# Performance work log

Measured on AMD Instinct MI355X. Metric: run time of the kernel, lower is better.

Reference implementation:

```python
import jax, jax.numpy as jnp
import numpy as np

H = 8  # num_heads


def setup_inputs() -> dict:
    key = jax.random.key(0)
    ks = jax.random.split(key, 8)
    B, N, C = 2048, 64, 256  # B = batch(8) * nW(256) windows, N = window tokens, C = dim
    nW = 256
    return {
        "x": jax.random.normal(ks[0], (B, N, C), jnp.float32),
        "mask": jax.random.normal(ks[1], (nW, N, N), jnp.float32),
        "Wq": jax.random.normal(ks[2], (C, C), jnp.float32) * (C ** -0.5),
        "bq": jax.random.normal(ks[3], (C,), jnp.float32) * 0.02,
        "Wkv": jax.random.normal(ks[4], (C, 2 * C), jnp.float32) * (C ** -0.5),
        "bkv": jax.random.normal(ks[5], (2 * C,), jnp.float32) * 0.02,
        "Wp": jax.random.normal(ks[6], (C, C), jnp.float32) * (C ** -0.5),
        "bp": jax.random.normal(ks[7], (C,), jnp.float32) * 0.02,
    }


def reference(x, mask, Wq, bq, Wkv, bkv, Wp, bp):
    B, N, C = x.shape
    dh = C // H
    scale = dh ** -0.5
    # projections (attn_kv is None -> self-attention)
    q = (x @ Wq + bq).reshape(B, N, H, dh).transpose(0, 2, 1, 3)          # [B,H,N,dh]
    kv = (x @ Wkv + bkv).reshape(B, N, 2, H, dh).transpose(2, 0, 3, 1, 4)  # [2,B,H,N,dh]
    k, v = kv[0], kv[1]
    attn = jnp.einsum("bhqd,bhkd->bhqk", q * scale, k)                    # [B,H,N,N]
    nW = mask.shape[0]
    attn = attn.reshape(B // nW, nW, H, N, N) + mask[None, :, None]
    attn = attn.reshape(B, H, N, N)
    attn = jax.nn.softmax(attn, axis=-1)
    out = jnp.einsum("bhqk,bhkd->bhqd", attn, v)                          # [B,H,N,dh]
    out = out.transpose(0, 2, 1, 3).reshape(B, N, C)
    return out @ Wp + bp
```

## Files before the change

kernel.cpp:

```cpp
#include <hip/hip_runtime.h>

typedef __bf16 bf16v8 __attribute__((ext_vector_type(8)));
typedef bf16v8 bf16x8 __attribute__((may_alias));
typedef unsigned int u32v2 __attribute__((ext_vector_type(2)));
typedef u32v2 u32x2 __attribute__((may_alias));
typedef unsigned short u16v8 __attribute__((ext_vector_type(8)));
typedef u16v8 u16x8 __attribute__((may_alias));
typedef unsigned short u16v;
typedef u16v u16 __attribute__((may_alias));
typedef _Float16 f16v4 __attribute__((ext_vector_type(4)));
typedef f16v4 f16x4 __attribute__((may_alias));
typedef _Float16 f16v;
typedef f16v f16s __attribute__((may_alias));
typedef float f32x4 __attribute__((ext_vector_type(4)));
typedef unsigned int u32;

#define MEMFENCE() asm volatile("" ::: "memory")

union B8 { u32 u[4]; bf16v8 v; };

__device__ __forceinline__ u32 cvtpk(float lo, float hi) {
    u32 r;
    asm("v_cvt_pk_bf16_f32 %0, %1, %2" : "=v"(r) : "v"(lo), "v"(hi));
    return r;
}

__device__ __forceinline__ unsigned short f2b(float f) {
    union { float f; unsigned u; } a; a.f = f;
    unsigned r = a.u + 0x7FFFu + ((a.u >> 16) & 1u);
    return (unsigned short)(r >> 16);
}

__global__ void prep_weights(const float* __restrict__ Wq,
                             const float* __restrict__ Wkv,
                             const float* __restrict__ Wp,
                             const float* __restrict__ bq,
                             const float* __restrict__ bkv,
                             u16* __restrict__ wt,
                             u16* __restrict__ wpt,
                             float* __restrict__ b_all)
{
    int idx = blockIdx.x * 256 + threadIdx.x;
    if (idx < 196608) {
        int h  = idx / 24576;   int r  = idx % 24576;
        int m  = r / 8192;      int r2 = r % 8192;
        int tj = r2 / 4096;     int r3 = r2 % 4096;
        int ks = r3 / 512;      int r4 = r3 % 512;
        int lane = r4 >> 3, j = r4 & 7;
        int o = h * 32 + tj * 16 + (lane & 15);
        int k = ks * 32 + (lane >> 4) * 8 + j;
        float v = (m == 0) ? Wq[k * 256 + o]
                           : Wkv[k * 512 + (m == 1 ? o : 256 + o)];
        wt[idx] = f2b(v);
    } else if (idx < 262144) {
        int f  = idx - 196608;
        int h  = f / 8192;      int r2 = f % 8192;
        int tj = r2 / 4096;     int r3 = r2 % 4096;
        int ks = r3 / 512;      int r4 = r3 % 512;
        int lane = r4 >> 3, j = r4 & 7;
        int o = h * 32 + tj * 16 + (lane & 15);
        int k = ks * 32 + (lane >> 4) * 8 + j;
        wpt[f] = f2b(Wp[k * 256 + o]);
    } else if (idx < 262912) {
        int i = idx - 262144;
        b_all[i] = (i < 256) ? bq[i] : bkv[i - 256];
    }
}

__global__ __launch_bounds__(512, 2)
void qkv_proj(const float* __restrict__ x,
              const u16* __restrict__ wt,
              const float* __restrict__ b_all,
              u16* __restrict__ qkv)
{
    __shared__ __align__(16) unsigned char smem[32768];
    const int b   = blockIdx.x;
    const int tid = threadIdx.x;
    const int w   = tid >> 6;
    const int l   = tid & 63;
    const int lr  = l & 15;
    const int lg  = l >> 4;
    const int hc  = w * 32;

    f32x4 zero = {0.f, 0.f, 0.f, 0.f};

    {
        const float* xb = x + (size_t)b * 16384;
#pragma unroll
        for (int it = 0; it < 4; ++it) {
            int g   = it * 512 + tid;
            int row = g >> 5;
            int cg  = g & 31;
            const float4 f0 = *(const float4*)(xb + row * 256 + cg * 8);
            const float4 f1 = *(const float4*)(xb + row * 256 + cg * 8 + 4);
            u16v8 t;
            t[0] = f2b(f0.x); t[1] = f2b(f0.y); t[2] = f2b(f0.z); t[3] = f2b(f0.w);
            t[4] = f2b(f1.x); t[5] = f2b(f1.y); t[6] = f2b(f1.z); t[7] = f2b(f1.w);
            int off = row * 512 + ((cg * 16) ^ ((row & 7) << 4));
            *(u16x8*)(smem + off) = t;
        }
    }
    __syncthreads();

    u16* qb  = qkv + (((size_t)b * 8 + w) * 3) * 2048;
    u16* kb_ = qb + 2048;
    unsigned char* vb = (unsigned char*)(qb + 4096);
    const u16* whead = wt + (size_t)w * 24576;

#pragma unroll
    for (int hf = 0; hf < 2; ++hf) {
        f32x4 qa[2][2], ka[2][2], va[2][2];
#pragma unroll
        for (int t = 0; t < 2; ++t)
#pragma unroll
            for (int tj = 0; tj < 2; ++tj) { qa[t][tj] = zero; ka[t][tj] = zero; va[t][tj] = zero; }
#pragma unroll
        for (int ks = 0; ks < 8; ++ks) {
            bf16v8 af[2];
#pragma unroll
            for (int t = 0; t < 2; ++t) {
                int row = hf * 32 + t * 16 + lr;
                af[t] = *(const bf16x8*)(smem + row * 512 + ((ks * 64 + lg * 16) ^ ((row & 7) << 4)));
            }
            bf16v8 bwq[2], bwk[2], bwv[2];
#pragma unroll
            for (int tj = 0; tj < 2; ++tj) {
                const u16* wp0 = whead + tj * 4096 + ks * 512 + l * 8;
                bwq[tj] = *(const bf16x8*)(wp0);
                bwk[tj] = *(const bf16x8*)(wp0 + 8192);
                bwv[tj] = *(const bf16x8*)(wp0 + 16384);
            }
            __builtin_amdgcn_s_setprio(1);
#pragma unroll
            for (int tj = 0; tj < 2; ++tj)
#pragma unroll
                for (int t = 0; t < 2; ++t) {
                    qa[t][tj] = __builtin_amdgcn_mfma_f32_16x16x32_bf16(af[t], bwq[tj], qa[t][tj], 0, 0, 0);
                    ka[t][tj] = __builtin_amdgcn_mfma_f32_16x16x32_bf16(af[t], bwk[tj], ka[t][tj], 0, 0, 0);
                    va[t][tj] = __builtin_amdgcn_mfma_f32_16x16x32_bf16(af[t], bwv[tj], va[t][tj], 0, 0, 0);
                }
            __builtin_amdgcn_s_setprio(0);
        }
#pragma unroll
        for (int tj = 0; tj < 2; ++tj) {
            float bqv = b_all[hc + tj * 16 + lr];
            float bkr = b_all[256 + hc + tj * 16 + lr];
            float bvr = b_all[512 + hc + tj * 16 + lr];
#pragma unroll
            for (int t = 0; t < 2; ++t) {
#pragma unroll
                for (int e = 0; e < 4; ++e) {
                    int tok = hf * 32 + t * 16 + lg * 4 + e;
                    qb[tok * 32 + tj * 16 + lr]  = f2b(qa[t][tj][e] + bqv);
                    kb_[tok * 32 + tj * 16 + lr] = f2b(ka[t][tj][e] + bkr);
                }
                int dh   = tj * 16 + lr;
                int tok0 = hf * 32 + t * 16 + lg * 4;
                u32x2 pv2;
                pv2[0] = cvtpk(va[t][tj][0] + bvr, va[t][tj][1] + bvr);
                pv2[1] = cvtpk(va[t][tj][2] + bvr, va[t][tj][3] + bvr);
                *(u32x2*)(vb + dh * 128 + tok0 * 2) = pv2;
            }
        }
    }
}

__global__ __launch_bounds__(512, 4)
void attn_out(const u16* __restrict__ qkv,
              const float* __restrict__ mask,
              const u16* __restrict__ wpt,
              const float* __restrict__ bp,
              float* __restrict__ out)
{
    __shared__ __align__(16) unsigned char smem[40960];
    const int b   = blockIdx.x;
    const int wdw = b & 255;
    const int tid = threadIdx.x;
    const int w   = tid >> 6;
    const int l   = tid & 63;
    const int lr  = l & 15;
    const int lg  = l >> 4;
    const int chunk = w * 4096;
    const int moff  = 32768;
    const int hc    = w * 32;
    const float scale = 0.17677669529663687f;

    f32x4 zero = {0.f, 0.f, 0.f, 0.f};

    {
        const float* mb = mask + (size_t)wdw * 4096;
#pragma unroll
        for (int it = 0; it < 8; ++it) {
            int idx = it * 512 + tid;
            int q = idx >> 6, k = idx & 63;
            int colp = (k & 15) * 4 + (k >> 4);
            *(f16s*)(smem + moff + q * 128 + ((colp * 2) ^ ((q & 7) << 4)))
                = (_Float16)mb[idx];
        }
    }
    __syncthreads();

    const u16* qb  = qkv + (((size_t)b * 8 + w) * 3) * 2048;
    const u16* kb_ = qb + 2048;
    const unsigned char* vb = (const unsigned char*)(qb + 4096);

    bf16v8 aq[4], bk[4];
#pragma unroll
    for (int ti = 0; ti < 4; ++ti)
        aq[ti] = *(const bf16x8*)(qb + (ti * 16 + lr) * 32 + lg * 8);
#pragma unroll
    for (int tj = 0; tj < 4; ++tj)
        bk[tj] = *(const bf16x8*)(kb_ + (tj * 16 + lr) * 32 + lg * 8);

    f32x4 sH[4][4];
    __builtin_amdgcn_s_setprio(1);
#pragma unroll
    for (int ti = 0; ti < 4; ++ti)
#pragma unroll
        for (int tj = 0; tj < 4; ++tj)
            sH[ti][tj] = __builtin_amdgcn_mfma_f32_16x16x32_bf16(aq[ti], bk[tj], zero, 0, 0, 0);
    __builtin_amdgcn_s_setprio(0);

#pragma unroll
    for (int ti = 0; ti < 4; ++ti)
#pragma unroll
        for (int e = 0; e < 4; ++e) {
            int row = ti * 16 + lg * 4 + e;
            f16v4 mv = *(const f16x4*)(smem + moff + row * 128 + ((lr * 8) ^ ((row & 7) << 4)));
#pragma unroll
            for (int tj = 0; tj < 4; ++tj)
                sH[ti][tj][e] = sH[ti][tj][e] * scale + (float)mv[tj];
        }
    float inv[4][4];
#pragma unroll
    for (int ti = 0; ti < 4; ++ti)
#pragma unroll
        for (int e = 0; e < 4; ++e) {
            float v0 = sH[ti][0][e], v1 = sH[ti][1][e];
            float v2 = sH[ti][2][e], v3 = sH[ti][3][e];
            float m = fmaxf(fmaxf(v0, v1), fmaxf(v2, v3));
#pragma unroll
            for (int d = 1; d < 16; d <<= 1) m = fmaxf(m, __shfl_xor(m, d));
            v0 = __expf(v0 - m); v1 = __expf(v1 - m);
            v2 = __expf(v2 - m); v3 = __expf(v3 - m);
            float s = v0 + v1 + v2 + v3;
#pragma unroll
            for (int d = 1; d < 16; d <<= 1) s += __shfl_xor(s, d);
            inv[ti][e] = 1.0f / s;
            sH[ti][0][e] = v0; sH[ti][1][e] = v1;
            sH[ti][2][e] = v2; sH[ti][3][e] = v3;
        }
    u32 pkP[4][4][2];
#pragma unroll
    for (int ti = 0; ti < 4; ++ti)
#pragma unroll
        for (int tj = 0; tj < 4; ++tj) {
            pkP[ti][tj][0] = cvtpk(sH[ti][tj][0], sH[ti][tj][1]);
            pkP[ti][tj][1] = cvtpk(sH[ti][tj][2], sH[ti][tj][3]);
        }

    f32x4 oH[4][2];
#pragma unroll
    for (int ti = 0; ti < 4; ++ti)
#pragma unroll
        for (int tjv = 0; tjv < 2; ++tjv) oH[ti][tjv] = zero;
#pragma unroll
    for (int kb2 = 0; kb2 < 2; ++kb2) {
#pragma unroll
        for (int ti = 0; ti < 4; ++ti)
#pragma unroll
            for (int tjh = 0; tjh < 2; ++tjh) {
                int c2 = (tjh * 16 + lr) * 2;
#pragma unroll
                for (int ep = 0; ep < 2; ++ep) {
                    u32 u = pkP[ti][2 * kb2 + tjh][ep];
                    int q0 = ti * 16 + lg * 4 + ep * 2;
                    *(u16*)(smem + chunk + q0 * 64 + (c2 ^ (((q0 >> 1) & 3) << 4))) = (unsigned short)u;
                    *(u16*)(smem + chunk + (q0 + 1) * 64 + (c2 ^ ((((q0 + 1) >> 1) & 3) << 4))) = (unsigned short)(u >> 16);
                }
            }
        MEMFENCE();
        bf16v8 bv[2];
#pragma unroll
        for (int tjv = 0; tjv < 2; ++tjv) {
            int dh = tjv * 16 + lr;
            bv[tjv] = *(const bf16x8*)(vb + dh * 128 + kb2 * 64 + lg * 16);
        }
#pragma unroll
        for (int ti = 0; ti < 4; ++ti) {
            int row = ti * 16 + lr;
            bf16v8 ap = *(const bf16x8*)(smem + chunk + row * 64 + ((lg * 16) ^ (((row >> 1) & 3) << 4)));
            __builtin_amdgcn_s_setprio(1);
#pragma unroll
            for (int tjv = 0; tjv < 2; ++tjv)
                oH[ti][tjv] = __builtin_amdgcn_mfma_f32_16x16x32_bf16(ap, bv[tjv], oH[ti][tjv], 0, 0, 0);
            __builtin_amdgcn_s_setprio(0);
        }
        MEMFENCE();
    }
#pragma unroll
    for (int ti = 0; ti < 4; ++ti)
#pragma unroll
        for (int tjv = 0; tjv < 2; ++tjv)
#pragma unroll
            for (int e = 0; e < 4; ++e)
                oH[ti][tjv][e] *= inv[ti][e];

    __syncthreads();

#pragma unroll
    for (int ti = 0; ti < 4; ++ti)
#pragma unroll
        for (int tjv = 0; tjv < 2; ++tjv)
#pragma unroll
            for (int e = 0; e < 4; ++e) {
                int row = ti * 16 + lg * 4 + e;
                int cg  = hc + tjv * 16 + lr;
                *(u16*)(smem + row * 512 + ((cg * 2) ^ ((row & 7) << 4)))
                    = f2b(oH[ti][tjv][e]);
            }
    __syncthreads();

    f32x4 pacc[4][2];
#pragma unroll
    for (int ti = 0; ti < 4; ++ti)
#pragma unroll
        for (int tj = 0; tj < 2; ++tj) pacc[ti][tj] = zero;
#pragma unroll
    for (int ks = 0; ks < 8; ++ks) {
        bf16v8 a_[4];
#pragma unroll
        for (int ti = 0; ti < 4; ++ti) {
            int row = ti * 16 + lr;
            a_[ti] = *(const bf16x8*)(smem + row * 512 + ((ks * 64 + lg * 16) ^ ((row & 7) << 4)));
        }
        bf16v8 bw[2];
#pragma unroll
        for (int tj = 0; tj < 2; ++tj)
            bw[tj] = *(const bf16x8*)(wpt + (size_t)w * 8192 + tj * 4096 + ks * 512 + l * 8);
        __builtin_amdgcn_s_setprio(1);
#pragma unroll
        for (int tj = 0; tj < 2; ++tj)
#pragma unroll
            for (int ti = 0; ti < 4; ++ti)
                pacc[ti][tj] = __builtin_amdgcn_mfma_f32_16x16x32_bf16(a_[ti], bw[tj], pacc[ti][tj], 0, 0, 0);
        __builtin_amdgcn_s_setprio(0);
    }
    float* ob = out + (size_t)b * 16384;
#pragma unroll
    for (int tj = 0; tj < 2; ++tj) {
        float bias = bp[hc + tj * 16 + lr];
#pragma unroll
        for (int ti = 0; ti < 4; ++ti)
#pragma unroll
            for (int e = 0; e < 4; ++e) {
                int row = ti * 16 + lg * 4 + e;
                ob[row * 256 + hc + tj * 16 + lr] = pacc[ti][tj][e] + bias;
            }
    }
}

extern "C" void kernel_launch(void* const* d_in, const int* in_sizes, int n_in,
                              void* d_out, int out_size, void* d_ws, size_t ws_size,
                              hipStream_t stream) {
    const float* x    = (const float*)d_in[0];
    const float* mask = (const float*)d_in[1];
    const float* Wq   = (const float*)d_in[2];
    const float* bq   = (const float*)d_in[3];
    const float* Wkv  = (const float*)d_in[4];
    const float* bkv  = (const float*)d_in[5];
    const float* Wp   = (const float*)d_in[6];
    const float* bp   = (const float*)d_in[7];
    float* out = (float*)d_out;

    u16*   wt    = (u16*)d_ws;
    u16*   wpt   = wt + 196608;
    float* b_all = (float*)(wpt + 65536);

    const size_t qkv_off   = 589824;
    u16* qkv = (u16*)((unsigned char*)d_ws + qkv_off);

    prep_weights<<<1027, 256, 0, stream>>>(Wq, Wkv, Wp, bq, bkv, wt, wpt, b_all);
    qkv_proj<<<2048, 512, 0, stream>>>(x, wt, b_all, qkv);
    attn_out<<<2048, 512, 0, stream>>>(qkv, mask, wpt, bp, out);
}
```

Measured before the change: 229.1 us.

## Process two windows per block in QKV projection to reuse weight fragments

Each qkv_proj block now handles two windows, stages both in 64KB of shared memory, and loops over Q/K/V matrices so that each weight fragment loaded from global memory is reused across both windows. The grid is halved to 1024 blocks. This halves the global weight traffic per window and keeps fewer accumulators live per matrix pass. In exchange it doubles LDS use per block, which limits occupancy, and the kernel has fewer blocks.

After: 202.6 us. -11.5%, faster.

```diff
diff --git a/kernel.cpp b/kernel.cpp
--- a/kernel.cpp
+++ b/kernel.cpp
@@ -73,8 +73,8 @@
               const float* __restrict__ b_all,
               u16* __restrict__ qkv)
 {
-    __shared__ __align__(16) unsigned char smem[32768];
-    const int b   = blockIdx.x;
+    __shared__ __align__(16) unsigned char smem[65536];
+    const int b0  = blockIdx.x * 2;
     const int tid = threadIdx.x;
     const int w   = tid >> 6;
     const int l   = tid & 63;
@@ -84,82 +84,81 @@
 
     f32x4 zero = {0.f, 0.f, 0.f, 0.f};
 
-    {
-        const float* xb = x + (size_t)b * 16384;
-#pragma unroll
-        for (int it = 0; it < 4; ++it) {
-            int g   = it * 512 + tid;
-            int row = g >> 5;
-            int cg  = g & 31;
-            const float4 f0 = *(const float4*)(xb + row * 256 + cg * 8);
-            const float4 f1 = *(const float4*)(xb + row * 256 + cg * 8 + 4);
-            u16v8 t;
-            t[0] = f2b(f0.x); t[1] = f2b(f0.y); t[2] = f2b(f0.z); t[3] = f2b(f0.w);
-            t[4] = f2b(f1.x); t[5] = f2b(f1.y); t[6] = f2b(f1.z); t[7] = f2b(f1.w);
-            int off = row * 512 + ((cg * 16) ^ ((row & 7) << 4));
-            *(u16x8*)(smem + off) = t;
-        }
+#pragma unroll
+    for (int it = 0; it < 8; ++it) {
+        int g   = it * 512 + tid;
+        int win = g >> 11;
+        int r2  = g & 2047;
+        int row = r2 >> 5;
+        int cg  = r2 & 31;
+        const float* xb = x + (size_t)(b0 + win) * 16384;
+        const float4 f0 = *(const float4*)(xb + row * 256 + cg * 8);
+        const float4 f1 = *(const float4*)(xb + row * 256 + cg * 8 + 4);
+        u16v8 t;
+        t[0] = f2b(f0.x); t[1] = f2b(f0.y); t[2] = f2b(f0.z); t[3] = f2b(f0.w);
+        t[4] = f2b(f1.x); t[5] = f2b(f1.y); t[6] = f2b(f1.z); t[7] = f2b(f1.w);
+        int off = win * 32768 + row * 512 + ((cg * 16) ^ ((row & 7) << 4));
+        *(u16x8*)(smem + off) = t;
     }
     __syncthreads();
 
-    u16* qb  = qkv + (((size_t)b * 8 + w) * 3) * 2048;
-    u16* kb_ = qb + 2048;
-    unsigned char* vb = (unsigned char*)(qb + 4096);
     const u16* whead = wt + (size_t)w * 24576;
 
 #pragma unroll
     for (int hf = 0; hf < 2; ++hf) {
-        f32x4 qa[2][2], ka[2][2], va[2][2];
-#pragma unroll
-        for (int t = 0; t < 2; ++t)
-#pragma unroll
-            for (int tj = 0; tj < 2; ++tj) { qa[t][tj] = zero; ka[t][tj] = zero; va[t][tj] = zero; }
-#pragma unroll
-        for (int ks = 0; ks < 8; ++ks) {
-            bf16v8 af[2];
-#pragma unroll
-            for (int t = 0; t < 2; ++t) {
-                int row = hf * 32 + t * 16 + lr;
-                af[t] = *(const bf16x8*)(smem + row * 512 + ((ks * 64 + lg * 16) ^ ((row & 7) << 4)));
-            }
-            bf16v8 bwq[2], bwk[2], bwv[2];
-#pragma unroll
-            for (int tj = 0; tj < 2; ++tj) {
-                const u16* wp0 = whead + tj * 4096 + ks * 512 + l * 8;
-                bwq[tj] = *(const bf16x8*)(wp0);
-                bwk[tj] = *(const bf16x8*)(wp0 + 8192);
-                bwv[tj] = *(const bf16x8*)(wp0 + 16384);
-            }
-            __builtin_amdgcn_s_setprio(1);
-#pragma unroll
-            for (int tj = 0; tj < 2; ++tj)
-#pragma unroll
-                for (int t = 0; t < 2; ++t) {
-                    qa[t][tj] = __builtin_amdgcn_mfma_f32_16x16x32_bf16(af[t], bwq[tj], qa[t][tj], 0, 0, 0);
-                    ka[t][tj] = __builtin_amdgcn_mfma_f32_16x16x32_bf16(af[t], bwk[tj], ka[t][tj], 0, 0, 0);
-                    va[t][tj] = __builtin_amdgcn_mfma_f32_16x16x32_bf16(af[t], bwv[tj], va[t][tj], 0, 0, 0);
+#pragma unroll
+        for (int m = 0; m < 3; ++m) {
+            f32x4 acc[2][2][2];
+#pragma unroll
+            for (int win = 0; win < 2; ++win)
+#pragma unroll
+                for (int t = 0; t < 2; ++t)
+#pragma unroll
+                    for (int tj = 0; tj < 2; ++tj) acc[win][t][tj] = zero;
+#pragma unroll
+            for (int ks = 0; ks < 8; ++ks) {
+                bf16v8 wf[2];
+#pragma unroll
+                for (int tj = 0; tj < 2; ++tj)
+                    wf[tj] = *(const bf16x8*)(whead + m * 8192 + tj * 4096 + ks * 512 + l * 8);
+#pragma unroll
+                for (int win = 0; win < 2; ++win)
+#pragma unroll
+                    for (int t = 0; t < 2; ++t) {
+                        int row = hf * 32 + t * 16 + lr;
+                        bf16v8 af = *(const bf16x8*)(smem + win * 32768 + row * 512 +
+                                                     ((ks * 64 + lg * 16) ^ ((row & 7) << 4)));
+                        __builtin_amdgcn_s_setprio(1);
+#pragma unroll
+                        for (int tj = 0; tj < 2; ++tj)
+                            acc[win][t][tj] = __builtin_amdgcn_mfma_f32_16x16x32_bf16(af, wf[tj], acc[win][t][tj], 0, 0, 0);
+                        __builtin_amdgcn_s_setprio(0);
+                    }
+            }
+#pragma unroll
+            for (int win = 0; win < 2; ++win) {
+                u16* base = qkv + (((size_t)(b0 + win) * 8 + w) * 3) * 2048 + m * 2048;
+#pragma unroll
+                for (int tj = 0; tj < 2; ++tj) {
+                    float bias = b_all[m * 256 + hc + tj * 16 + lr];
+#pragma unroll
+                    for (int t = 0; t < 2; ++t) {
+                        if (m < 2) {
+#pragma unroll
+                            for (int e = 0; e < 4; ++e) {
+                                int tok = hf * 32 + t * 16 + lg * 4 + e;
+                                base[tok * 32 + tj * 16 + lr] = f2b(acc[win][t][tj][e] + bias);
+                            }
+                        } else {
+                            int dh   = tj * 16 + lr;
+                            int tok0 = hf * 32 + t * 16 + lg * 4;
+                            u32x2 pv2;
+                            pv2[0] = cvtpk(acc[win][t][tj][0] + bias, acc[win][t][tj][1] + bias);
+                            pv2[1] = cvtpk(acc[win][t][tj][2] + bias, acc[win][t][tj][3] + bias);
+                            *(u32x2*)((unsigned char*)base + dh * 128 + tok0 * 2) = pv2;
+                        }
+                    }
                 }
-            __builtin_amdgcn_s_setprio(0);
-        }
-#pragma unroll
-        for (int tj = 0; tj < 2; ++tj) {
-            float bqv = b_all[hc + tj * 16 + lr];
-            float bkr = b_all[256 + hc + tj * 16 + lr];
-            float bvr = b_all[512 + hc + tj * 16 + lr];
-#pragma unroll
-            for (int t = 0; t < 2; ++t) {
-#pragma unroll
-                for (int e = 0; e < 4; ++e) {
-                    int tok = hf * 32 + t * 16 + lg * 4 + e;
-                    qb[tok * 32 + tj * 16 + lr]  = f2b(qa[t][tj][e] + bqv);
-                    kb_[tok * 32 + tj * 16 + lr] = f2b(ka[t][tj][e] + bkr);
-                }
-                int dh   = tj * 16 + lr;
-                int tok0 = hf * 32 + t * 16 + lg * 4;
-                u32x2 pv2;
-                pv2[0] = cvtpk(va[t][tj][0] + bvr, va[t][tj][1] + bvr);
-                pv2[1] = cvtpk(va[t][tj][2] + bvr, va[t][tj][3] + bvr);
-                *(u32x2*)(vb + dh * 128 + tok0 * 2) = pv2;
             }
         }
     }
@@ -381,6 +380,6 @@
     u16* qkv = (u16*)((unsigned char*)d_ws + qkv_off);
 
     prep_weights<<<1027, 256, 0, stream>>>(Wq, Wkv, Wp, bq, bkv, wt, wpt, b_all);
-    qkv_proj<<<2048, 512, 0, stream>>>(x, wt, b_all, qkv);
+    qkv_proj<<<1024, 512, 0, stream>>>(x, wt, b_all, qkv);
     attn_out<<<2048, 512, 0, stream>>>(qkv, mask, wpt, bp, out);
 }
```
